# Kernel optimization log

Measured on AMD Instinct MI355X. Metric: run time of the kernel, lower is better.

Reference implementation:

```python
import jax, jax.numpy as jnp
import numpy as np

N, E, D, R, NB, ARD, L, G, NS = 50000, 600000, 128, 200, 4, 32, 2, 50, 2000
ATT_IN = 2 * D + 2 * ARD  # 320


def setup_inputs() -> dict:
    key = jax.random.key(0)
    ks = jax.random.split(key, 20)
    node_feat = jax.random.normal(ks[0], (N, D), jnp.float32)
    total_edge = jax.random.randint(ks[1], (2, E), 0, N, jnp.int32)
    total_relation = jax.random.randint(ks[2], (E,), 0, R, jnp.int32)
    total_relation_embed = jax.random.normal(ks[3], (E, ARD), jnp.float32)
    total_target_relation = jax.random.normal(ks[4], (E, ARD), jnp.float32)
    source_node = jax.random.randint(ks[5], (NS,), 0, N, jnp.int32)
    target_node = jax.random.randint(ks[6], (NS,), 0, N, jnp.int32)
    # 50 equal-size contiguous graphs (matches graph_sizes slicing in original)
    graph_ids = ((jnp.arange(N) * G) // N).astype(jnp.int32)
    s = 1.0 / np.sqrt(D)
    weights = jax.random.normal(ks[7], (L, NB, D, D), jnp.float32) * s
    w_comps = jax.random.normal(ks[8], (L, R, NB), jnp.float32) * (1.0 / np.sqrt(NB))
    self_loops = jax.random.normal(ks[9], (L, D, D), jnp.float32) * s
    A_w = jax.random.normal(ks[10], (L, D, ATT_IN), jnp.float32) * (1.0 / np.sqrt(ATT_IN))
    A_b = jnp.zeros((L, D), jnp.float32)
    B_w = jax.random.normal(ks[11], (L, 1, D), jnp.float32) * s
    B_b = jnp.zeros((L, 1), jnp.float32)
    return dict(node_feat=node_feat, total_edge=total_edge, total_relation=total_relation,
                total_relation_embed=total_relation_embed,
                total_target_relation=total_target_relation,
                source_node=source_node, target_node=target_node, graph_ids=graph_ids,
                weights=weights, w_comps=w_comps, self_loops=self_loops,
                A_w=A_w, A_b=A_b, B_w=B_w, B_b=B_b)


def _layer(x, src, tgt, rel, rel_embed, tgt_rel, weight, w_comp, self_loop, A_w, A_b, B_w, B_b):
    # basis-decomposed per-relation message: msg_e = x[src_e] @ (sum_b w_comp[rel_e,b] * weight_b)
    x_src = x[src]                      # (E, D) gather
    x_tgt = x[tgt]                      # (E, D) gather
    coef = w_comp[rel]                  # (E, NB)
    msg = jnp.einsum('ei,eb,bio->eo', x_src, coef, weight)  # (E, D)
    curr = x @ self_loop                # (N, D) self-loop
    # attention MLP over [src, tgt, rel_embed, target_rel]
    e_feat = jnp.concatenate([x_src, x_tgt, rel_embed, tgt_rel], axis=1)  # (E, 320)
    h = jax.nn.relu(e_feat @ A_w.T + A_b)
    a = jax.nn.sigmoid(h @ B_w.T + B_b)  # (E, 1)
    attn_msg = jax.ops.segment_sum(msg * a, tgt, num_segments=N)  # e2n_sp scatter-add
    # propagate's relu followed by layer activation relu (idempotent)
    return jax.nn.relu(curr + attn_msg)


def reference(node_feat, total_edge, total_relation, total_relation_embed,
              total_target_relation, source_node, target_node, graph_ids,
              weights, w_comps, self_loops, A_w, A_b, B_w, B_b):
    src, tgt = total_edge[0], total_edge[1]
    x = node_feat
    feats = []
    for l in range(L):
        x = _layer(x, src, tgt, total_relation, total_relation_embed,
                   total_target_relation, weights[l], w_comps[l], self_loops[l],
                   A_w[l], A_b[l], B_w[l], B_b[l])
        feats.append(x)
    total = jnp.concatenate(feats, axis=1)  # (N, L*D)
    source_embed = total[source_node]
    target_embed = total[target_node]
    counts = jax.ops.segment_sum(jnp.ones((N,), total.dtype), graph_ids, num_segments=G)
    graph_embed = jax.ops.segment_sum(total, graph_ids, num_segments=G) / counts[:, None]
    return graph_embed, source_embed, target_embed
```

## Files before the change

### kernel.cpp

```cpp
#include <hip/hip_runtime.h>


#define NN 50000
#define NP 50048
#define EE 600000
#define DD 128
#define RR 200
#define NBASIS 4
#define LL 2
#define GG 50
#define NSRC 2000
#define GCH 8

typedef __attribute__((ext_vector_type(8))) short short8v;
typedef __attribute__((ext_vector_type(4))) float float4v;
typedef __attribute__((ext_vector_type(8))) _Float16 half8v;
typedef __attribute__((ext_vector_type(4))) _Float16 half4v;

__device__ __forceinline__ void f4a(const float4 v, float* a) {
  a[0] = v.x; a[1] = v.y; a[2] = v.z; a[3] = v.w;
}

__device__ __forceinline__ unsigned short f2bf(float v) {
  unsigned u = __float_as_uint(v);
  unsigned r = u + 0x7FFFu + ((u >> 16) & 1u);
  return (unsigned short)(r >> 16);
}
__device__ __forceinline__ float bf2f(unsigned short h) {
  return __uint_as_float(((unsigned)h) << 16);
}

__device__ __forceinline__ void split8s(const float4 a, const float4 b,
                                        short8v* hi, short8v* lo) {
  float f[8];
  f4a(a, f); f4a(b, f + 4);
  short8v h, l;
#pragma unroll
  for (int j = 0; j < 8; ++j) {
    unsigned short hh = f2bf(f[j]);
    h[j] = (short)hh;
    l[j] = (short)f2bf(f[j] - bf2f(hh));
  }
  *hi = h; *lo = l;
}

__global__ __launch_bounds__(256) void k_bigwT(const float* __restrict__ weights,
                                               const float* __restrict__ A_w,
                                               const float* __restrict__ self_loops,
                                               unsigned short* __restrict__ BThi,
                                               unsigned short* __restrict__ BTlo, int l) {
  int id = blockIdx.x * 256 + threadIdx.x;
  if (id >= 128 * 896) return;
  int i = id / 896, c = id % 896;
  float v;
  if (c < 512) {
    int b = c >> 7, o = c & 127;
    v = weights[((l * NBASIS + b) * DD + i) * DD + o];
  } else if (c < 640) {
    int j = c - 512;
    v = A_w[(l * DD + j) * 320 + i];
  } else if (c < 768) {
    int j = c - 640;
    v = A_w[(l * DD + j) * 320 + 128 + i];
  } else {
    int o = c - 768;
    v = self_loops[(l * DD + i) * DD + o];
  }
  unsigned short hi = f2bf(v);
  unsigned short lo = f2bf(v - bf2f(hi));
  BThi[c * 128 + i] = hi;
  BTlo[c * 128 + i] = lo;
}

__global__ __launch_bounds__(256) void k_qw(const float* __restrict__ A_w,
                                            unsigned short* __restrict__ QWhi,
                                            unsigned short* __restrict__ QWlo, int l) {
  int id = blockIdx.x * 256 + threadIdx.x;
  if (id >= 128 * 64) return;
  int j = id >> 6, k = id & 63;
  float v = A_w[(l * DD + j) * 320 + 256 + k];
  unsigned short hi = f2bf(v);
  QWhi[id] = hi;
  QWlo[id] = f2bf(v - bf2f(hi));
}

__global__ __launch_bounds__(256) void k_prepE(const int* __restrict__ eord,
                                               const float* __restrict__ re,
                                               const float* __restrict__ tr,
                                               unsigned short* __restrict__ ECh) {
  int id = blockIdx.x * 256 + threadIdx.x;
  if (id >= EE * 4) return;
  int p = id >> 2, kb = (id & 3) * 8;
  int eid = eord[p];
  float4 r0 = *(const float4*)&re[(size_t)eid * 32 + kb];
  float4 r1 = *(const float4*)&re[(size_t)eid * 32 + kb + 4];
  float4 t0 = *(const float4*)&tr[(size_t)eid * 32 + kb];
  float4 t1 = *(const float4*)&tr[(size_t)eid * 32 + kb + 4];
  unsigned short* ep = ECh + (size_t)p * 128;
  short8v h, lo;
  split8s(r0, r1, &h, &lo);
  *(short8v*)(ep + kb) = h;
  *(short8v*)(ep + 64 + kb) = lo;
  split8s(t0, t1, &h, &lo);
  *(short8v*)(ep + 32 + kb) = h;
  *(short8v*)(ep + 96 + kb) = lo;
}

__global__ __launch_bounds__(256) void k_splitX(const float* __restrict__ X, int xs,
                                                unsigned short* __restrict__ Xhi,
                                                unsigned short* __restrict__ Xlo) {
  int id = blockIdx.x * 256 + threadIdx.x;
  if (id >= NP * 128) return;
  int n = id >> 7, k = id & 127;
  float v = (n < NN) ? X[(size_t)n * xs + k] : 0.0f;
  unsigned short hi = f2bf(v);
  unsigned short lo = f2bf(v - bf2f(hi));
  Xhi[id] = hi;
  Xlo[id] = lo;
}

__global__ __launch_bounds__(256) void k_mgemm(const unsigned short* __restrict__ Xhi,
                                               const unsigned short* __restrict__ Xlo,
                                               const unsigned short* __restrict__ BThi,
                                               const unsigned short* __restrict__ BTlo,
                                               _Float16* __restrict__ xw16,
                                               _Float16* __restrict__ pst16,
                                               float* __restrict__ currdst) {
  __shared__ __align__(16) char smem[34816];
  unsigned short* sBhi = (unsigned short*)smem;
  unsigned short* sBlo = sBhi + 128 * 56;
  _Float16* sC = (_Float16*)smem;
  float* sCf = (float*)smem;

  const int t = threadIdx.x;
  const int wv = t >> 6, lane = t & 63;
  const int lm = lane & 15, qd = lane >> 4;
  const int m0 = blockIdx.x * 128;
  const int cb = blockIdx.y;
  const int n0 = cb * 128;
  const int mw = m0 + wv * 32;

  float4v acc[2][8];
#pragma unroll
  for (int mi = 0; mi < 2; ++mi)
#pragma unroll
    for (int nt = 0; nt < 8; ++nt) acc[mi][nt] = (float4v)(0.0f);

  const int sn = (t >> 2);
  const int skq = (t & 3) * 8;

  for (int kc = 0; kc < 128; kc += 32) {
    short8v vh0 = *(const short8v*)(BThi + (size_t)(n0 + sn) * 128 + kc + skq);
    short8v vl0 = *(const short8v*)(BTlo + (size_t)(n0 + sn) * 128 + kc + skq);
    short8v vh1 = *(const short8v*)(BThi + (size_t)(n0 + 64 + sn) * 128 + kc + skq);
    short8v vl1 = *(const short8v*)(BTlo + (size_t)(n0 + 64 + sn) * 128 + kc + skq);
    if (kc) __syncthreads();
    *(short8v*)&sBhi[sn * 56 + skq] = vh0;
    *(short8v*)&sBlo[sn * 56 + skq] = vl0;
    *(short8v*)&sBhi[(64 + sn) * 56 + skq] = vh1;
    *(short8v*)&sBlo[(64 + sn) * 56 + skq] = vl1;
    __syncthreads();
    short8v ah[2], al[2];
#pragma unroll
    for (int mi = 0; mi < 2; ++mi) {
      ah[mi] = *(const short8v*)(Xhi + (size_t)(mw + mi * 16 + lm) * 128 + kc + qd * 8);
      al[mi] = *(const short8v*)(Xlo + (size_t)(mw + mi * 16 + lm) * 128 + kc + qd * 8);
    }
#pragma unroll
    for (int nt = 0; nt < 8; ++nt) {
      short8v bh = *(const short8v*)&sBhi[(nt * 16 + lm) * 56 + qd * 8];
      short8v bl = *(const short8v*)&sBlo[(nt * 16 + lm) * 56 + qd * 8];
#pragma unroll
      for (int mi = 0; mi < 2; ++mi) {
        acc[mi][nt] = __builtin_amdgcn_mfma_f32_16x16x32_bf16(ah[mi], bh, acc[mi][nt], 0, 0, 0);
        acc[mi][nt] = __builtin_amdgcn_mfma_f32_16x16x32_bf16(ah[mi], bl, acc[mi][nt], 0, 0, 0);
        acc[mi][nt] = __builtin_amdgcn_mfma_f32_16x16x32_bf16(al[mi], bh, acc[mi][nt], 0, 0, 0);
      }
    }
  }

  if (cb < 6) {
    _Float16* dst16; int stride, off;
    if (cb < 4) { dst16 = xw16;  stride = 512; off = cb * 128; }
    else        { dst16 = pst16; stride = 256; off = (cb - 4) * 128; }
    __syncthreads();
#pragma unroll
    for (int mi = 0; mi < 2; ++mi)
#pragma unroll
      for (int nt = 0; nt < 8; ++nt)
#pragma unroll
        for (int r = 0; r < 4; ++r) {
          int col = (cb < 4) ? (nt * 16 + lm) : ((lm >> 2) * 32 + nt * 4 + (lm & 3));
          sC[(wv * 32 + mi * 16 + qd * 4 + r) * 136 + col] = (_Float16)acc[mi][nt][r];
        }
    __syncthreads();
#pragma unroll
    for (int rep = 0; rep < 8; ++rep) {
      int idx = rep * 256 + t;
      int row = idx >> 4, li = idx & 15;
      int m = m0 + row;
      if (m < NN)
        *(half8v*)&dst16[(size_t)m * stride + off + li * 8] =
            *(const half8v*)&sC[row * 136 + li * 8];
    }
  } else {
#pragma unroll
    for (int pass = 0; pass < 2; ++pass) {
      __syncthreads();
      if ((wv >> 1) == pass) {
        int rbase = (wv & 1) * 32;
#pragma unroll
        for (int mi = 0; mi < 2; ++mi)
#pragma unroll
          for (int nt = 0; nt < 8; ++nt)
#pragma unroll
            for (int r = 0; r < 4; ++r)
              sCf[(rbase + mi * 16 + qd * 4 + r) * 132 + nt * 16 + lm] = acc[mi][nt][r];
      }
      __syncthreads();
#pragma unroll
      for (int rep = 0; rep < 8; ++rep) {
        int idx = rep * 256 + t;
        int lr = idx >> 5, li = idx & 31;
        int m = m0 + pass * 64 + lr;
        if (m < NN)
          *(float4*)&currdst[(size_t)m * 256 + li * 4] =
              *(const float4*)&sCf[lr * 132 + li * 4];
      }
    }
  }
}

template <bool PRE>
__global__ __launch_bounds__(256, 5) void k_attn(
    const int* __restrict__ srcs, const int* __restrict__ tgtc,
    const int* __restrict__ relc, const int* __restrict__ eord,
    const float* __restrict__ re, const float* __restrict__ tr,
    const unsigned short* __restrict__ ECh,
    const unsigned short* __restrict__ QWhi, const unsigned short* __restrict__ QWlo,
    const float* __restrict__ A_b, const float* __restrict__ B_w,
    const float* __restrict__ B_b, const float* __restrict__ w_comps,
    const _Float16* __restrict__ pst16, float* __restrict__ acf, int l) {
  __shared__ __align__(16) unsigned short sQW[2 * 8192];
  const int t = threadIdx.x;

#pragma unroll
  for (int r = 0; r < 4; ++r) {
    int idx = r * 256 + t;
    int ad = (idx * 16) ^ (((idx >> 3) & 7) << 4);
    *(short8v*)((char*)sQW + ad) = *(const short8v*)(QWhi + idx * 8);
    *(short8v*)((char*)sQW + 16384 + ad) = *(const short8v*)(QWlo + idx * 8);
  }

  const int wv = t >> 6, lane = t & 63;
  const int lm = lane & 15, qd = lane >> 4;
  const int p = blockIdx.x * 64 + wv * 16 + lm;
  const int src = srcs[p], tgt = tgtc[p];

  short8v eh0, el0, eh1, el1;
  if constexpr (PRE) {
    const unsigned short* ep = ECh + (size_t)p * 128;
    eh0 = *(const short8v*)(ep + qd * 8);
    eh1 = *(const short8v*)(ep + 32 + qd * 8);
    el0 = *(const short8v*)(ep + 64 + qd * 8);
    el1 = *(const short8v*)(ep + 96 + qd * 8);
  } else {
    const int eid = eord[p];
    float4 r0 = *(const float4*)&re[(size_t)eid * 32 + qd * 8];
    float4 r1 = *(const float4*)&re[(size_t)eid * 32 + qd * 8 + 4];
    float4 t0 = *(const float4*)&tr[(size_t)eid * 32 + qd * 8];
    float4 t1 = *(const float4*)&tr[(size_t)eid * 32 + qd * 8 + 4];
    split8s(r0, r1, &eh0, &el0);
    split8s(t0, t1, &eh1, &el1);
  }

  half8v psA[4], ptA[4];
  {
    const _Float16* psp = pst16 + (size_t)src * 256 + qd * 32;
    const _Float16* ptp = pst16 + (size_t)tgt * 256 + 128 + qd * 32;
#pragma unroll
    for (int i = 0; i < 4; ++i) {
      psA[i] = *(const half8v*)(psp + i * 8);
      ptA[i] = *(const half8v*)(ptp + i * 8);
    }
  }

  __syncthreads();

  float4v acc[8];
#pragma unroll
  for (int nt = 0; nt < 8; ++nt) acc[nt] = (float4v)(0.0f);
  const int sw = (lm & 7) << 4;
#pragma unroll
  for (int nt = 0; nt < 8; ++nt) {
    const int rowb = (nt * 16 + lm) * 128 + qd * 16;
    short8v wh0 = *(const short8v*)((char*)sQW + (rowb ^ sw));
    short8v wh1 = *(const short8v*)((char*)sQW + ((rowb + 64) ^ sw));
    short8v wl0 = *(const short8v*)((char*)sQW + 16384 + (rowb ^ sw));
    short8v wl1 = *(const short8v*)((char*)sQW + 16384 + ((rowb + 64) ^ sw));
    acc[nt] = __builtin_amdgcn_mfma_f32_16x16x32_bf16(wh0, eh0, acc[nt], 0, 0, 0);
    acc[nt] = __builtin_amdgcn_mfma_f32_16x16x32_bf16(wl0, eh0, acc[nt], 0, 0, 0);
    acc[nt] = __builtin_amdgcn_mfma_f32_16x16x32_bf16(wh0, el0, acc[nt], 0, 0, 0);
    acc[nt] = __builtin_amdgcn_mfma_f32_16x16x32_bf16(wh1, eh1, acc[nt], 0, 0, 0);
    acc[nt] = __builtin_amdgcn_mfma_f32_16x16x32_bf16(wl1, eh1, acc[nt], 0, 0, 0);
    acc[nt] = __builtin_amdgcn_mfma_f32_16x16x32_bf16(wh1, el1, acc[nt], 0, 0, 0);
  }

  float part = 0.0f;
#pragma unroll
  for (int nt = 0; nt < 8; ++nt) {
    float4 ab = *(const float4*)&A_b[l * DD + nt * 16 + qd * 4];
    float4 bw = *(const float4*)&B_w[l * DD + nt * 16 + qd * 4];
    float abv[4], bwv[4];
    f4a(ab, abv); f4a(bw, bwv);
#pragma unroll
    for (int r = 0; r < 4; ++r) {
      float ps = (float)psA[nt >> 1][(nt & 1) * 4 + r];
      float pt = (float)ptA[nt >> 1][(nt & 1) * 4 + r];
      float h = fmaxf(ps + pt + acc[nt][r] + abv[r], 0.0f);
      part += h * bwv[r];
    }
  }
  part += __shfl_xor(part, 16, 64);
  part += __shfl_xor(part, 32, 64);
  if (qd == 0) {
    const float a = 1.0f / (1.0f + expf(-(part + B_b[l])));
    const float4 cf = *(const float4*)&w_comps[(l * RR + relc[p]) * 4];
    *(float4*)&acf[(size_t)p * 4] = make_float4(a * cf.x, a * cf.y, a * cf.z, a * cf.w);
  }
}

__global__ __launch_bounds__(256) void k_zero_i(int* __restrict__ p, int n) {
  int id = blockIdx.x * 256 + threadIdx.x;
  if (id < n) p[id] = 0;
}
__global__ __launch_bounds__(256) void k_hist(const int* __restrict__ e_tgt,
                                              int* __restrict__ deg) {
  int e = blockIdx.x * 256 + threadIdx.x;
  if (e < EE) atomicAdd(&deg[e_tgt[e]], 1);
}
__global__ __launch_bounds__(1024) void k_scan(const int* __restrict__ deg,
                                               int* __restrict__ rowptr,
                                               int* __restrict__ cursor) {
  __shared__ int part[1024];
  const int t = threadIdx.x;
  const int chunk = (NN + 1023) / 1024;
  int lo = t * chunk, hi = min(lo + chunk, NN);
  int s = 0;
  for (int i = lo; i < hi; ++i) s += deg[i];
  part[t] = s;
  __syncthreads();
  for (int off = 1; off < 1024; off <<= 1) {
    int v = (t >= off) ? part[t - off] : 0;
    __syncthreads();
    part[t] += v;
    __syncthreads();
  }
  int run = (t == 0) ? 0 : part[t - 1];
  for (int i = lo; i < hi; ++i) {
    int d = deg[i];
    rowptr[i] = run; cursor[i] = run;
    run += d;
  }
  if (t == 0) rowptr[NN] = EE;
}
__global__ __launch_bounds__(256) void k_fill(const int* __restrict__ e_tgt,
                                              const int* __restrict__ e_src,
                                              const int* __restrict__ rel,
                                              int* __restrict__ cursor,
                                              int* __restrict__ srcs,
                                              int* __restrict__ eord,
                                              int* __restrict__ relc,
                                              int* __restrict__ tgtc) {
  int e = blockIdx.x * 256 + threadIdx.x;
  if (e < EE) {
    int tg = e_tgt[e];
    int p = atomicAdd(&cursor[tg], 1);
    srcs[p] = e_src[e];
    eord[p] = e;
    relc[p] = rel[e];
    tgtc[p] = tg;
  }
}

__global__ __launch_bounds__(256) void k_reduce(
    const int* __restrict__ rowptr, const int* __restrict__ srcs,
    const float* __restrict__ acf, const _Float16* __restrict__ xw16,
    float* __restrict__ feats, int l) {
  const int t = threadIdx.x;
  const int wave = t >> 6, lane = t & 63;
  const int n = blockIdx.x * 4 + wave;
  if (n >= NN) return;
  const int b = lane >> 4, li = lane & 15;
  float s[8] = {0, 0, 0, 0, 0, 0, 0, 0};
  const int lo = rowptr[n], hi = rowptr[n + 1];
  int snext = 0; float cnext = 0.0f;
  if (lo < hi) { snext = srcs[lo]; cnext = acf[lo * 4 + b]; }
  for (int i = lo; i < hi; ++i) {
    const int src = snext; const float cb_ = cnext;
    if (i + 1 < hi) { snext = srcs[i + 1]; cnext = acf[(i + 1) * 4 + b]; }
    half8v x = *(const half8v*)&xw16[(size_t)src * 512 + b * 128 + li * 8];
#pragma unroll
    for (int j = 0; j < 8; ++j) s[j] += cb_ * (float)x[j];
  }
#pragma unroll
  for (int j = 0; j < 8; ++j) {
    s[j] += __shfl_xor(s[j], 16, 64);
    s[j] += __shfl_xor(s[j], 32, 64);
  }
  if (lane < 16) {
    float* fp = &feats[(size_t)n * 256 + l * 128 + lane * 8];
    float4 c0 = *(const float4*)fp;
    float4 c1 = *(const float4*)(fp + 4);
    float4 o0 = make_float4(fmaxf(s[0] + c0.x, 0.f), fmaxf(s[1] + c0.y, 0.f),
                            fmaxf(s[2] + c0.z, 0.f), fmaxf(s[3] + c0.w, 0.f));
    float4 o1 = make_float4(fmaxf(s[4] + c1.x, 0.f), fmaxf(s[5] + c1.y, 0.f),
                            fmaxf(s[6] + c1.z, 0.f), fmaxf(s[7] + c1.w, 0.f));
    *(float4*)fp = o0;
    *(float4*)(fp + 4) = o1;
  }
}

__global__ __launch_bounds__(256) void k_gather(const int* __restrict__ srcn,
                                                const int* __restrict__ tgtn,
                                                const float* __restrict__ feats,
                                                float* __restrict__ out) {
  int id = blockIdx.x * 256 + threadIdx.x;
  if (id >= 2 * NSRC * 256) return;
  int half = id / (NSRC * 256);
  int rem = id % (NSRC * 256);
  int s = rem >> 8, c = rem & 255;
  int n = half ? tgtn[s] : srcn[s];
  int base = GG * 256 + half * NSRC * 256;
  out[base + s * 256 + c] = feats[n * 256 + c];
}

__global__ __launch_bounds__(256) void k_zero(float* __restrict__ p, int n) {
  int id = blockIdx.x * 256 + threadIdx.x;
  if (id < n) p[id] = 0.0f;
}

__global__ __launch_bounds__(256) void k_graphsum(const int* __restrict__ gid,
                                                  const float* __restrict__ feats,
                                                  float* __restrict__ gsum,
                                                  float* __restrict__ gcnt) {
  const int g = blockIdx.x / GCH, ch = blockIdx.x % GCH;
  __shared__ int sb[2];
  if (threadIdx.x == 0) {
    int lo = 0, hi = NN;
    while (lo < hi) { int m = (lo + hi) >> 1; if (gid[m] < g) lo = m + 1; else hi = m; }
    sb[0] = lo;
    lo = 0; hi = NN;
    while (lo < hi) { int m = (lo + hi) >> 1; if (gid[m] < g + 1) lo = m + 1; else hi = m; }
    sb[1] = lo;
  }
  __syncthreads();
  const int lo = sb[0], hi = sb[1];
  if (ch == 0 && threadIdx.x == 0) gcnt[g] = (float)(hi - lo);
  const int cnt = hi - lo;
  const int per = (cnt + GCH - 1) / GCH;
  const int nlo = lo + ch * per, nhi = min(nlo + per, hi);
  float s = 0.0f;
  const int c = threadIdx.x;
  for (int n = nlo; n < nhi; ++n) s += feats[n * 256 + c];
  atomicAdd(&gsum[g * 256 + c], s);
}

__global__ __launch_bounds__(256) void k_graphdiv(const float* __restrict__ gsum,
                                                  const float* __restrict__ gcnt,
                                                  float* __restrict__ out) {
  int id = blockIdx.x * 256 + threadIdx.x;
  if (id >= GG * 256) return;
  out[id] = gsum[id] / gcnt[id >> 8];
}

extern "C" void kernel_launch(void* const* d_in, const int* in_sizes, int n_in,
                              void* d_out, int out_size, void* d_ws, size_t ws_size,
                              hipStream_t stream) {
  const float* node_feat  = (const float*)d_in[0];
  const int*   edge       = (const int*)d_in[1];
  const int*   rel        = (const int*)d_in[2];
  const float* re         = (const float*)d_in[3];
  const float* tr         = (const float*)d_in[4];
  const int*   srcn       = (const int*)d_in[5];
  const int*   tgtn       = (const int*)d_in[6];
  const int*   gid        = (const int*)d_in[7];
  const float* weights    = (const float*)d_in[8];
  const float* w_comps    = (const float*)d_in[9];
  const float* self_loops = (const float*)d_in[10];
  const float* A_w        = (const float*)d_in[11];
  const float* A_b        = (const float*)d_in[12];
  const float* B_w        = (const float*)d_in[13];
  const float* B_b        = (const float*)d_in[14];
  float* out = (float*)d_out;

  float* ws    = (float*)d_ws;
  float* feats = ws;
  float* gsum  = feats + (size_t)NN * 256;
  float* gcnt  = gsum + GG * 256;
  float* acf   = gcnt + 64;
  _Float16* xw16  = (_Float16*)(acf + (size_t)EE * 4);
  _Float16* pst16 = xw16 + (size_t)NN * 512;
  unsigned short* Xhi  = (unsigned short*)(pst16 + (size_t)NN * 256);
  unsigned short* Xlo  = Xhi + (size_t)NP * 128;
  unsigned short* BThi = Xlo + (size_t)NP * 128;
  unsigned short* BTlo = BThi + 896 * 128;
  int* deg    = (int*)(BTlo + 896 * 128);
  int* rowptr = deg + NN;
  int* cursor = rowptr + NN + 1;
  int* srcs   = cursor + NN;
  int* eord   = srcs + EE;
  int* relc   = eord + EE;
  int* tgtc   = relc + EE;
  unsigned short* QWhi = (unsigned short*)(tgtc + EE);
  unsigned short* QWlo = QWhi + 128 * 64;
  unsigned short* ECh  = QWlo + 128 * 64;
  const size_t needed = (size_t)((char*)(ECh + (size_t)EE * 128) - (char*)d_ws);
  const bool pre = ws_size >= needed;

  const int* e_src = edge;
  const int* e_tgt = edge + EE;

  k_zero_i<<<(NN + 255) / 256, 256, 0, stream>>>(deg, NN);
  k_hist<<<(EE + 255) / 256, 256, 0, stream>>>(e_tgt, deg);
  k_scan<<<1, 1024, 0, stream>>>(deg, rowptr, cursor);
  k_fill<<<(EE + 255) / 256, 256, 0, stream>>>(e_tgt, e_src, rel, cursor,
                                               srcs, eord, relc, tgtc);
  if (pre)
    k_prepE<<<(EE * 4 + 255) / 256, 256, 0, stream>>>(eord, re, tr, ECh);

  for (int l = 0; l < LL; ++l) {
    const float* X = (l == 0) ? node_feat : feats;
    int xs = (l == 0) ? 128 : 256;
    k_bigwT<<<(128 * 896 + 255) / 256, 256, 0, stream>>>(weights, A_w, self_loops,
                                                         BThi, BTlo, l);
    k_qw<<<(128 * 64 + 255) / 256, 256, 0, stream>>>(A_w, QWhi, QWlo, l);
    k_splitX<<<(NP * 128 + 255) / 256, 256, 0, stream>>>(X, xs, Xhi, Xlo);
    dim3 g1(NP / 128, 7);
    k_mgemm<<<g1, 256, 0, stream>>>(Xhi, Xlo, BThi, BTlo, xw16, pst16, feats + l * 128);
    if (pre)
      k_attn<true><<<EE / 64, 256, 0, stream>>>(srcs, tgtc, relc, eord, re, tr, ECh,
                                                QWhi, QWlo, A_b, B_w, B_b, w_comps,
                                                pst16, acf, l);
    else
      k_attn<false><<<EE / 64, 256, 0, stream>>>(srcs, tgtc, relc, eord, re, tr, ECh,
                                                 QWhi, QWlo, A_b, B_w, B_b, w_comps,
                                                 pst16, acf, l);
    k_reduce<<<(NN + 3) / 4, 256, 0, stream>>>(rowptr, srcs, acf, xw16, feats, l);
  }
  k_gather<<<(2 * NSRC * 256 + 255) / 256, 256, 0, stream>>>(srcn, tgtn, feats, out);
  k_zero<<<(GG * 256 + 64 + 255) / 256, 256, 0, stream>>>(gsum, GG * 256 + 64);
  k_graphsum<<<GG * GCH, 256, 0, stream>>>(gid, feats, gsum, gcnt);
  k_graphdiv<<<GG, 256, 0, stream>>>(gsum, gcnt, out);
}
```

Before: 976.0 us.

## Make attention kernel persistent with software-prefetched edge data, drop precomputed split

Drops the precomputed bf16 hi/lo edge-feature buffer and its prep kernel. The attention kernel now runs as a persistent grid of 768 blocks in which each wave walks strided 16-edge chunks. It prefetches the next chunk's relation and target-relation vectors and the indices two chunks ahead, so gather latency overlaps the MFMA work. This avoids the prep kernel's write and re-read of a large buffer, at the cost of redoing the float-to-bf16 split per layer, higher register pressure (launch bounds lowered to 3 blocks), and reading the relation and target-relation data through eord indirection.

```diff
diff --git a/kernel.cpp b/kernel.cpp
--- a/kernel.cpp
+++ b/kernel.cpp
@@ -11,6 +11,7 @@
 #define GG 50
 #define NSRC 2000
 #define GCH 8
+#define ATTN_BLOCKS 768
 
 typedef __attribute__((ext_vector_type(8))) short short8v;
 typedef __attribute__((ext_vector_type(4))) float float4v;
@@ -84,28 +85,6 @@
   QWlo[id] = f2bf(v - bf2f(hi));
 }
 
-__global__ __launch_bounds__(256) void k_prepE(const int* __restrict__ eord,
-                                               const float* __restrict__ re,
-                                               const float* __restrict__ tr,
-                                               unsigned short* __restrict__ ECh) {
-  int id = blockIdx.x * 256 + threadIdx.x;
-  if (id >= EE * 4) return;
-  int p = id >> 2, kb = (id & 3) * 8;
-  int eid = eord[p];
-  float4 r0 = *(const float4*)&re[(size_t)eid * 32 + kb];
-  float4 r1 = *(const float4*)&re[(size_t)eid * 32 + kb + 4];
-  float4 t0 = *(const float4*)&tr[(size_t)eid * 32 + kb];
-  float4 t1 = *(const float4*)&tr[(size_t)eid * 32 + kb + 4];
-  unsigned short* ep = ECh + (size_t)p * 128;
-  short8v h, lo;
-  split8s(r0, r1, &h, &lo);
-  *(short8v*)(ep + kb) = h;
-  *(short8v*)(ep + 64 + kb) = lo;
-  split8s(t0, t1, &h, &lo);
-  *(short8v*)(ep + 32 + kb) = h;
-  *(short8v*)(ep + 96 + kb) = lo;
-}
-
 __global__ __launch_bounds__(256) void k_splitX(const float* __restrict__ X, int xs,
                                                 unsigned short* __restrict__ Xhi,
                                                 unsigned short* __restrict__ Xlo) {
@@ -231,12 +210,10 @@
   }
 }
 
-template <bool PRE>
-__global__ __launch_bounds__(256, 5) void k_attn(
+__global__ __launch_bounds__(256, 3) void k_attn(
     const int* __restrict__ srcs, const int* __restrict__ tgtc,
     const int* __restrict__ relc, const int* __restrict__ eord,
     const float* __restrict__ re, const float* __restrict__ tr,
-    const unsigned short* __restrict__ ECh,
     const unsigned short* __restrict__ QWhi, const unsigned short* __restrict__ QWlo,
     const float* __restrict__ A_b, const float* __restrict__ B_w,
     const float* __restrict__ B_b, const float* __restrict__ w_comps,
@@ -254,79 +231,110 @@
 
   const int wv = t >> 6, lane = t & 63;
   const int lm = lane & 15, qd = lane >> 4;
-  const int p = blockIdx.x * 64 + wv * 16 + lm;
-  const int src = srcs[p], tgt = tgtc[p];
-
-  short8v eh0, el0, eh1, el1;
-  if constexpr (PRE) {
-    const unsigned short* ep = ECh + (size_t)p * 128;
-    eh0 = *(const short8v*)(ep + qd * 8);
-    eh1 = *(const short8v*)(ep + 32 + qd * 8);
-    el0 = *(const short8v*)(ep + 64 + qd * 8);
-    el1 = *(const short8v*)(ep + 96 + qd * 8);
-  } else {
-    const int eid = eord[p];
-    float4 r0 = *(const float4*)&re[(size_t)eid * 32 + qd * 8];
-    float4 r1 = *(const float4*)&re[(size_t)eid * 32 + qd * 8 + 4];
-    float4 t0 = *(const float4*)&tr[(size_t)eid * 32 + qd * 8];
-    float4 t1 = *(const float4*)&tr[(size_t)eid * 32 + qd * 8 + 4];
-    split8s(r0, r1, &eh0, &el0);
-    split8s(t0, t1, &eh1, &el1);
-  }
-
-  half8v psA[4], ptA[4];
-  {
-    const _Float16* psp = pst16 + (size_t)src * 256 + qd * 32;
-    const _Float16* ptp = pst16 + (size_t)tgt * 256 + 128 + qd * 32;
-#pragma unroll
-    for (int i = 0; i < 4; ++i) {
-      psA[i] = *(const half8v*)(psp + i * 8);
-      ptA[i] = *(const half8v*)(ptp + i * 8);
-    }
+  const int NW = gridDim.x * 4;
+  const int NC = EE / 16;
+  const int c0 = blockIdx.x * 4 + wv;
+  const float Bb = B_b[l];
+  const int sw = (lm & 7) << 4;
+
+  int sA = 0, tA = 0, eA = 0, rA = 0;
+  int sB = 0, tB = 0, eB = 0, rB = 0;
+  float4 r0A, r1A, t0A, t1A;
+  r0A = r1A = t0A = t1A = make_float4(0.f, 0.f, 0.f, 0.f);
+
+  if (c0 < NC) {
+    int p = c0 * 16 + lm;
+    sA = srcs[p]; tA = tgtc[p]; eA = eord[p]; rA = relc[p];
+    r0A = *(const float4*)&re[(size_t)eA * 32 + qd * 8];
+    r1A = *(const float4*)&re[(size_t)eA * 32 + qd * 8 + 4];
+    t0A = *(const float4*)&tr[(size_t)eA * 32 + qd * 8];
+    t1A = *(const float4*)&tr[(size_t)eA * 32 + qd * 8 + 4];
+  }
+  if (c0 + NW < NC) {
+    int p = (c0 + NW) * 16 + lm;
+    sB = srcs[p]; tB = tgtc[p]; eB = eord[p]; rB = relc[p];
   }
 
   __syncthreads();
 
-  float4v acc[8];
-#pragma unroll
-  for (int nt = 0; nt < 8; ++nt) acc[nt] = (float4v)(0.0f);
-  const int sw = (lm & 7) << 4;
-#pragma unroll
-  for (int nt = 0; nt < 8; ++nt) {
-    const int rowb = (nt * 16 + lm) * 128 + qd * 16;
-    short8v wh0 = *(const short8v*)((char*)sQW + (rowb ^ sw));
-    short8v wh1 = *(const short8v*)((char*)sQW + ((rowb + 64) ^ sw));
-    short8v wl0 = *(const short8v*)((char*)sQW + 16384 + (rowb ^ sw));
-    short8v wl1 = *(const short8v*)((char*)sQW + 16384 + ((rowb + 64) ^ sw));
-    acc[nt] = __builtin_amdgcn_mfma_f32_16x16x32_bf16(wh0, eh0, acc[nt], 0, 0, 0);
-    acc[nt] = __builtin_amdgcn_mfma_f32_16x16x32_bf16(wl0, eh0, acc[nt], 0, 0, 0);
-    acc[nt] = __builtin_amdgcn_mfma_f32_16x16x32_bf16(wh0, el0, acc[nt], 0, 0, 0);
-    acc[nt] = __builtin_amdgcn_mfma_f32_16x16x32_bf16(wh1, eh1, acc[nt], 0, 0, 0);
-    acc[nt] = __builtin_amdgcn_mfma_f32_16x16x32_bf16(wl1, eh1, acc[nt], 0, 0, 0);
-    acc[nt] = __builtin_amdgcn_mfma_f32_16x16x32_bf16(wh1, el1, acc[nt], 0, 0, 0);
-  }
-
-  float part = 0.0f;
-#pragma unroll
-  for (int nt = 0; nt < 8; ++nt) {
-    float4 ab = *(const float4*)&A_b[l * DD + nt * 16 + qd * 4];
-    float4 bw = *(const float4*)&B_w[l * DD + nt * 16 + qd * 4];
-    float abv[4], bwv[4];
-    f4a(ab, abv); f4a(bw, bwv);
-#pragma unroll
-    for (int r = 0; r < 4; ++r) {
-      float ps = (float)psA[nt >> 1][(nt & 1) * 4 + r];
-      float pt = (float)ptA[nt >> 1][(nt & 1) * 4 + r];
-      float h = fmaxf(ps + pt + acc[nt][r] + abv[r], 0.0f);
-      part += h * bwv[r];
-    }
-  }
-  part += __shfl_xor(part, 16, 64);
-  part += __shfl_xor(part, 32, 64);
-  if (qd == 0) {
-    const float a = 1.0f / (1.0f + expf(-(part + B_b[l])));
-    const float4 cf = *(const float4*)&w_comps[(l * RR + relc[p]) * 4];
-    *(float4*)&acf[(size_t)p * 4] = make_float4(a * cf.x, a * cf.y, a * cf.z, a * cf.w);
+  for (int c = c0; c < NC; c += NW) {
+    const int cn = c + NW, cnn = c + 2 * NW;
+
+    half8v psA[4], ptA[4];
+    {
+      const _Float16* psp = pst16 + (size_t)sA * 256 + qd * 32;
+      const _Float16* ptp = pst16 + (size_t)tA * 256 + 128 + qd * 32;
+#pragma unroll
+      for (int i = 0; i < 4; ++i) {
+        psA[i] = *(const half8v*)(psp + i * 8);
+        ptA[i] = *(const half8v*)(ptp + i * 8);
+      }
+    }
+
+    float4 r0B, r1B, t0B, t1B;
+    r0B = r1B = t0B = t1B = make_float4(0.f, 0.f, 0.f, 0.f);
+    if (cn < NC) {
+      r0B = *(const float4*)&re[(size_t)eB * 32 + qd * 8];
+      r1B = *(const float4*)&re[(size_t)eB * 32 + qd * 8 + 4];
+      t0B = *(const float4*)&tr[(size_t)eB * 32 + qd * 8];
+      t1B = *(const float4*)&tr[(size_t)eB * 32 + qd * 8 + 4];
+    }
+
+    int sN = 0, tN = 0, eN = 0, rN = 0;
+    if (cnn < NC) {
+      int p = cnn * 16 + lm;
+      sN = srcs[p]; tN = tgtc[p]; eN = eord[p]; rN = relc[p];
+    }
+
+    short8v eh0, el0, eh1, el1;
+    split8s(r0A, r1A, &eh0, &el0);
+    split8s(t0A, t1A, &eh1, &el1);
+
+    float4v acc[8];
+#pragma unroll
+    for (int nt = 0; nt < 8; ++nt) acc[nt] = (float4v)(0.0f);
+#pragma unroll
+    for (int nt = 0; nt < 8; ++nt) {
+      const int rowb = (nt * 16 + lm) * 128 + qd * 16;
+      short8v wh0 = *(const short8v*)((char*)sQW + (rowb ^ sw));
+      short8v wh1 = *(const short8v*)((char*)sQW + ((rowb + 64) ^ sw));
+      short8v wl0 = *(const short8v*)((char*)sQW + 16384 + (rowb ^ sw));
+      short8v wl1 = *(const short8v*)((char*)sQW + 16384 + ((rowb + 64) ^ sw));
+      acc[nt] = __builtin_amdgcn_mfma_f32_16x16x32_bf16(wh0, eh0, acc[nt], 0, 0, 0);
+      acc[nt] = __builtin_amdgcn_mfma_f32_16x16x32_bf16(wl0, eh0, acc[nt], 0, 0, 0);
+      acc[nt] = __builtin_amdgcn_mfma_f32_16x16x32_bf16(wh0, el0, acc[nt], 0, 0, 0);
+      acc[nt] = __builtin_amdgcn_mfma_f32_16x16x32_bf16(wh1, eh1, acc[nt], 0, 0, 0);
+      acc[nt] = __builtin_amdgcn_mfma_f32_16x16x32_bf16(wl1, eh1, acc[nt], 0, 0, 0);
+      acc[nt] = __builtin_amdgcn_mfma_f32_16x16x32_bf16(wh1, el1, acc[nt], 0, 0, 0);
+    }
+
+    float part = 0.0f;
+#pragma unroll
+    for (int nt = 0; nt < 8; ++nt) {
+      float4 ab = *(const float4*)&A_b[l * DD + nt * 16 + qd * 4];
+      float4 bw = *(const float4*)&B_w[l * DD + nt * 16 + qd * 4];
+      float abv[4], bwv[4];
+      f4a(ab, abv); f4a(bw, bwv);
+#pragma unroll
+      for (int r = 0; r < 4; ++r) {
+        float ps = (float)psA[nt >> 1][(nt & 1) * 4 + r];
+        float pt = (float)ptA[nt >> 1][(nt & 1) * 4 + r];
+        float h = fmaxf(ps + pt + acc[nt][r] + abv[r], 0.0f);
+        part += h * bwv[r];
+      }
+    }
+    part += __shfl_xor(part, 16, 64);
+    part += __shfl_xor(part, 32, 64);
+    if (qd == 0) {
+      const float a = 1.0f / (1.0f + expf(-(part + Bb)));
+      const float4 cf = *(const float4*)&w_comps[(l * RR + rA) * 4];
+      *(float4*)&acf[(size_t)(c * 16 + lm) * 4] =
+          make_float4(a * cf.x, a * cf.y, a * cf.z, a * cf.w);
+    }
+
+    sA = sB; tA = tB; eA = eB; rA = rB;
+    r0A = r0B; r1A = r1B; t0A = t0B; t1A = t1B;
+    sB = sN; tB = tN; eB = eN; rB = rN;
   }
 }
 
@@ -514,9 +522,6 @@
   int* tgtc   = relc + EE;
   unsigned short* QWhi = (unsigned short*)(tgtc + EE);
   unsigned short* QWlo = QWhi + 128 * 64;
-  unsigned short* ECh  = QWlo + 128 * 64;
-  const size_t needed = (size_t)((char*)(ECh + (size_t)EE * 128) - (char*)d_ws);
-  const bool pre = ws_size >= needed;
 
   const int* e_src = edge;
   const int* e_tgt = edge + EE;
@@ -526,8 +531,6 @@
   k_scan<<<1, 1024, 0, stream>>>(deg, rowptr, cursor);
   k_fill<<<(EE + 255) / 256, 256, 0, stream>>>(e_tgt, e_src, rel, cursor,
                                                srcs, eord, relc, tgtc);
-  if (pre)
-    k_prepE<<<(EE * 4 + 255) / 256, 256, 0, stream>>>(eord, re, tr, ECh);
 
   for (int l = 0; l < LL; ++l) {
     const float* X = (l == 0) ? node_feat : feats;
@@ -538,14 +541,9 @@
     k_splitX<<<(NP * 128 + 255) / 256, 256, 0, stream>>>(X, xs, Xhi, Xlo);
     dim3 g1(NP / 128, 7);
     k_mgemm<<<g1, 256, 0, stream>>>(Xhi, Xlo, BThi, BTlo, xw16, pst16, feats + l * 128);
-    if (pre)
-      k_attn<true><<<EE / 64, 256, 0, stream>>>(srcs, tgtc, relc, eord, re, tr, ECh,
-                                                QWhi, QWlo, A_b, B_w, B_b, w_comps,
-                                                pst16, acf, l);
-    else
-      k_attn<false><<<EE / 64, 256, 0, stream>>>(srcs, tgtc, relc, eord, re, tr, ECh,
-                                                 QWhi, QWlo, A_b, B_w, B_b, w_comps,
-                                                 pst16, acf, l);
+    k_attn<<<ATTN_BLOCKS, 256, 0, stream>>>(srcs, tgtc, relc, eord, re, tr,
+                                            QWhi, QWlo, A_b, B_w, B_b, w_comps,
+                                            pst16, acf, l);
     k_reduce<<<(NN + 3) / 4, 256, 0, stream>>>(rowptr, srcs, acf, xw16, feats, l);
   }
   k_gather<<<(2 * NSRC * 256 + 255) / 256, 256, 0, stream>>>(srcn, tgtn, feats, out);
```

After: 1.311 ms. 34.3% more time.
